# Kernel optimization log

Measured on AMD Instinct MI355X. Metric: run time of the kernel, lower is better.

Reference implementation:

```python
import jax, jax.numpy as jnp
import numpy as np

B, NP, K, E = 8, 4096, 1024, 262144   # graphs, nodes/graph, topk keep, edges
N = B * NP
EPS = 1e-5


def _glorot(k, fi, fo):
    lim = float(np.sqrt(6.0 / (fi + fo)))
    return jax.random.uniform(k, (fi, fo), jnp.float32, -lim, lim)


def setup_inputs() -> dict:
    key = jax.random.key(0)
    ks = jax.random.split(key, 16)
    pos = jax.random.normal(ks[0], (N, 3), jnp.float32)
    epg = E // B
    src = jax.random.randint(ks[1], (E,), 0, NP)
    dst = jax.random.randint(ks[2], (E,), 0, NP)
    off = jnp.repeat(jnp.arange(B) * NP, epg)   # edges stay within their graph
    edge_index = jnp.stack([src + off, dst + off]).astype(jnp.int32)
    batch = jnp.repeat(jnp.arange(B, dtype=jnp.int32), NP)
    inp = {"pos": pos, "edge_index": edge_index, "batch": batch,
           "p": jax.random.normal(ks[3], (3,), jnp.float32)}
    dims = [3, 64, 128, 128, 256, 512]
    for i in range(5):
        fi, fo = dims[i], dims[i + 1]
        inp[f"W{i+1}"] = _glorot(ks[4 + i], fi, fo)
        inp[f"b{i+1}"] = jnp.zeros((fo,), jnp.float32)
        inp[f"g{i+1}"] = jnp.ones((fo,), jnp.float32)
        inp[f"be{i+1}"] = jnp.zeros((fo,), jnp.float32)
    for i, (fi, fo) in enumerate([(512, 256), (256, 256), (256, 100)]):
        inp[f"fw{i+1}"] = _glorot(ks[9 + i], fi, fo)
        inp[f"fb{i+1}"] = jnp.zeros((fo,), jnp.float32)
    return inp


def _bn(x, g, b):
    # BatchNorm1d in training mode: batch stats over the node dim
    m = jnp.mean(x, 0)
    v = jnp.var(x, 0)
    return (x - m) * jax.lax.rsqrt(v + EPS) * g + b


def _gcn(x, src, dst, ew, W, bb, n):
    # GCNConv with add_self_loops=True, symmetric normalization.
    h = x @ W                                              # [n, out]
    deg = jax.ops.segment_sum(ew, dst, num_segments=n) + 1.0  # +1 self-loop
    dinv = jax.lax.rsqrt(deg)
    norm = dinv[src] * ew * dinv[dst]                      # masked edges -> 0
    agg = jax.ops.segment_sum(h[src] * norm[:, None], dst, num_segments=n)
    return agg + h * (dinv * dinv)[:, None] + bb           # self-loop term + bias


def _forward(pos, p, W1, b1, g1, be1, W2, b2, g2, be2, W3, b3, g3, be3,
             W4, b4, g4, be4, W5, b5, g5, be5, fw1, fb1, fw2, fb2, fw3, fb3,
             edge_index):
    # --- TopKPooling(ratio=1024): projection score, tanh, top-k per graph ---
    s = jnp.tanh(pos @ p / jnp.linalg.norm(p))             # [N]
    vals, idx = jax.lax.top_k(s.reshape(B, NP), K)         # [B,K]
    perm = (idx + (jnp.arange(B) * NP)[:, None]).reshape(-1)
    x = pos[perm] * vals.reshape(-1)[:, None]              # gate kept nodes
    Nn = B * K
    remap = jnp.full((N,), -1, jnp.int32).at[perm].set(jnp.arange(Nn, dtype=jnp.int32))
    src, dst = remap[edge_index[0]], remap[edge_index[1]]
    valid = (src >= 0) & (dst >= 0)
    ew = valid.astype(x.dtype)                             # 0-weight == removed edge
    src = jnp.where(valid, src, 0)
    dst = jnp.where(valid, dst, 0)
    for (W, bb, g, be) in ((W1, b1, g1, be1), (W2, b2, g2, be2),
                           (W3, b3, g3, be3), (W4, b4, g4, be4),
                           (W5, b5, g5, be5)):
        x = jax.nn.relu(_bn(_gcn(x, src, dst, ew, W, bb, Nn), g, be))
    # --- global sum pooling (torch_scatter default reduce='sum') ---
    batch_new = jnp.repeat(jnp.arange(B), K)
    x = jax.ops.segment_sum(x, batch_new, num_segments=B)  # [B,512]
    x = jax.nn.relu(x @ fw1 + fb1)
    x = jax.nn.relu(x @ fw2 + fb2)
    return jax.nn.log_softmax(x @ fw3 + fb3, axis=-1)      # [B,100]


def reference(pos, edge_index, batch, p, W1, b1, g1, be1, W2, b2, g2, be2,
              W3, b3, g3, be3, W4, b4, g4, be4, W5, b5, g5, be5,
              fw1, fb1, fw2, fb2, fw3, fb3):
    del batch  # graph ids are the fixed contiguous layout encoded in B, NP, K
    return _forward(pos, p, W1, b1, g1, be1, W2, b2, g2, be2, W3, b3, g3, be3,
                    W4, b4, g4, be4, W5, b5, g5, be5,
                    fw1, fb1, fw2, fb2, fw3, fb3, edge_index)
```

## Files before the change

### kernel.cpp

```cpp
#include <hip/hip_runtime.h>
#include <math.h>

#define NTOT 32768
#define NPG  4096
#define BGR  8
#define KK   1024
#define NN   8192
#define NE   262144

typedef __attribute__((ext_vector_type(8))) short bf16x8;
typedef __attribute__((ext_vector_type(4))) float f32x4;

static __device__ __forceinline__ unsigned short f2bf(float f) {
    unsigned u = __float_as_uint(f);
    return (unsigned short)((u + 0x7fffu + ((u >> 16) & 1u)) >> 16);
}
static __device__ __forceinline__ float bf2f(unsigned short b) {
    return __uint_as_float(((unsigned)b) << 16);
}

__global__ void k_init(int* remap, int* deg, int* cursor) {
    int i = blockIdx.x * blockDim.x + threadIdx.x;
    if (i < NTOT) remap[i] = -1;
    if (i < NN) { deg[i] = 0; cursor[i] = 0; }
}

__global__ __launch_bounds__(1024) void k_topk2(const float* __restrict__ pos,
                                                const float* __restrict__ p,
                                                int* __restrict__ remap,
                                                float* __restrict__ x0f,
                                                unsigned short* __restrict__ Ab0) {
    __shared__ unsigned skey[NPG];
    __shared__ float sval[NPG];
    __shared__ int hist[256];
    __shared__ int Sarr[256];
    __shared__ int wsum[16];
    __shared__ int s_bin, s_above;

    const int g = blockIdx.x, tid = threadIdx.x;
    const int lane = tid & 63, wid = tid >> 6;
    const float p0 = p[0], p1 = p[1], p2 = p[2];
    const float invn = 1.0f / sqrtf(p0 * p0 + p1 * p1 + p2 * p2);

    for (int i = tid; i < NPG; i += 1024) {
        const float* pp = pos + (size_t)(g * NPG + i) * 3;
        float s = tanhf((pp[0] * p0 + pp[1] * p1 + pp[2] * p2) * invn);
        sval[i] = s;
        unsigned b = __float_as_uint(s);
        skey[i] = (b & 0x80000000u) ? ~b : (b | 0x80000000u);
    }
    __syncthreads();

    unsigned prefix = 0;
    int needed = KK;
    for (int r = 0; r < 4; ++r) {
        const int sh = 24 - 8 * r;
        if (tid < 256) hist[tid] = 0;
        __syncthreads();
        for (int i = tid; i < NPG; i += 1024) {
            unsigned k = skey[i];
            bool act = (r == 0) || ((k >> (sh + 8)) == prefix);
            if (act) atomicAdd(&hist[(k >> sh) & 255u], 1);
        }
        __syncthreads();
        if (wid == 0) {
            int h0 = hist[4 * lane + 0], h1 = hist[4 * lane + 1];
            int h2 = hist[4 * lane + 2], h3 = hist[4 * lane + 3];
            int l3 = h3, l2 = h2 + l3, l1 = h1 + l2, l0 = h0 + l1;
            int t = l0;
            for (int off = 1; off < 64; off <<= 1) {
                int n = __shfl_down(t, off, 64);
                if (lane + off < 64) t += n;
            }
            int hi = t - l0;
            Sarr[4 * lane + 0] = l0 + hi;
            Sarr[4 * lane + 1] = l1 + hi;
            Sarr[4 * lane + 2] = l2 + hi;
            Sarr[4 * lane + 3] = l3 + hi;
        }
        __syncthreads();
        if (tid < 256) {
            int Sb = Sarr[tid];
            int Sb1 = (tid < 255) ? Sarr[tid + 1] : 0;
            if (Sb >= needed && Sb1 < needed) { s_bin = tid; s_above = Sb1; }
        }
        __syncthreads();
        needed -= s_above;
        prefix = (prefix << 8) | (unsigned)s_bin;
        __syncthreads();
    }
    const unsigned Tkey = prefix;
    const int needTies = needed;

    int tiebase = 0, keepbase = 0;
    for (int c = 0; c < 4; ++c) {
        const int i = c * 1024 + tid;
        const unsigned k = skey[i];
        const int tie = (k == Tkey) ? 1 : 0;
        int v = tie;
        for (int off = 1; off < 64; off <<= 1) {
            int n = __shfl_up(v, off, 64);
            if (lane >= off) v += n;
        }
        if (lane == 63) wsum[wid] = v;
        __syncthreads();
        if (wid == 0) {
            int w = (lane < 16) ? wsum[lane] : 0;
            for (int off = 1; off < 16; off <<= 1) {
                int n = __shfl_up(w, off, 64);
                if (lane >= off) w += n;
            }
            if (lane < 16) wsum[lane] = w;
        }
        __syncthreads();
        const int trank = tiebase + v + (wid > 0 ? wsum[wid - 1] : 0) - tie;
        const int ttot = wsum[15];
        const int keep = (k > Tkey) || (tie && trank < needTies);
        __syncthreads();
        int u = keep;
        for (int off = 1; off < 64; off <<= 1) {
            int n = __shfl_up(u, off, 64);
            if (lane >= off) u += n;
        }
        if (lane == 63) wsum[wid] = u;
        __syncthreads();
        if (wid == 0) {
            int w = (lane < 16) ? wsum[lane] : 0;
            for (int off = 1; off < 16; off <<= 1) {
                int n = __shfl_up(w, off, 64);
                if (lane >= off) w += n;
            }
            if (lane < 16) wsum[lane] = w;
        }
        __syncthreads();
        const int kincl = u + (wid > 0 ? wsum[wid - 1] : 0);
        const int ktot = wsum[15];
        if (keep) {
            int nn = g * KK + keepbase + kincl - 1;
            remap[g * NPG + i] = nn;
            float val = sval[i];
            const float* pp = pos + (size_t)(g * NPG + i) * 3;
            float v0 = pp[0] * val, v1 = pp[1] * val, v2 = pp[2] * val;
            x0f[(size_t)nn * 3 + 0] = v0;
            x0f[(size_t)nn * 3 + 1] = v1;
            x0f[(size_t)nn * 3 + 2] = v2;
            unsigned short* rw = Ab0 + (size_t)nn * 32;
            ushort4 a = make_ushort4(f2bf(v0), f2bf(v1), f2bf(v2), 0);
            ushort4 z = make_ushort4(0, 0, 0, 0);
            *(ushort4*)(rw) = a;
#pragma unroll
            for (int t = 1; t < 8; ++t) *(ushort4*)(rw + 4 * t) = z;
        }
        tiebase += ttot;
        keepbase += ktot;
        __syncthreads();
    }
}

__global__ void k_deg(const int* __restrict__ ei, const int* __restrict__ remap,
                      int* __restrict__ deg) {
    int e = blockIdx.x * blockDim.x + threadIdx.x;
    if (e >= NE) return;
    int s = remap[ei[e]];
    int d = remap[ei[NE + e]];
    if (s >= 0 && d >= 0) atomicAdd(&deg[d], 1);
}

__global__ __launch_bounds__(1024) void k_scan(const int* __restrict__ deg,
                                               int* __restrict__ rowptr) {
    __shared__ int part[1024];
    const int tid = threadIdx.x;
    const int base = tid * 8;
    int loc[8];
    int s = 0;
#pragma unroll
    for (int i = 0; i < 8; ++i) { loc[i] = s; s += deg[base + i]; }
    part[tid] = s;
    __syncthreads();
    for (int off = 1; off < 1024; off <<= 1) {
        int v = (tid >= off) ? part[tid - off] : 0;
        __syncthreads();
        part[tid] += v;
        __syncthreads();
    }
    int pre = (tid > 0) ? part[tid - 1] : 0;
#pragma unroll
    for (int i = 0; i < 8; ++i) rowptr[base + i] = pre + loc[i];
    if (tid == 1023) rowptr[NN] = pre + s;
}

__global__ void k_place2(const int* __restrict__ ei, const int* __restrict__ remap,
                         const int* __restrict__ deg, const int* __restrict__ rowptr,
                         int* __restrict__ cursor, int* __restrict__ col,
                         float* __restrict__ ew) {
    int e = blockIdx.x * blockDim.x + threadIdx.x;
    if (e >= NE) return;
    int s = remap[ei[e]];
    int d = remap[ei[NE + e]];
    if (s >= 0 && d >= 0) {
        int pos = rowptr[d] + atomicAdd(&cursor[d], 1);
        col[pos] = s;
        ew[pos] = rsqrtf((float)(deg[s] + 1)) * rsqrtf((float)(deg[d] + 1));
    }
}

__global__ void k_wt_all(const float* __restrict__ w0, const float* __restrict__ w1,
                         const float* __restrict__ w2, const float* __restrict__ w3,
                         const float* __restrict__ w4,
                         unsigned short* __restrict__ t0, unsigned short* __restrict__ t1,
                         unsigned short* __restrict__ t2, unsigned short* __restrict__ t3,
                         unsigned short* __restrict__ t4) {
    int i = blockIdx.x * blockDim.x + threadIdx.x;
    const float* W; unsigned short* T; int Kd, Nc, Kpad, base;
    if (i < 2048)        { W = w0; T = t0; Kd = 3;   Nc = 64;  Kpad = 32;  base = 0; }
    else if (i < 10240)  { W = w1; T = t1; Kd = 64;  Nc = 128; Kpad = 64;  base = 2048; }
    else if (i < 26624)  { W = w2; T = t2; Kd = 128; Nc = 128; Kpad = 128; base = 10240; }
    else if (i < 59392)  { W = w3; T = t3; Kd = 128; Nc = 256; Kpad = 128; base = 26624; }
    else if (i < 190464) { W = w4; T = t4; Kd = 256; Nc = 512; Kpad = 256; base = 59392; }
    else return;
    int j = i - base;
    int n = j / Kpad, k = j - n * Kpad;
    float v = (k < Kd) ? W[(size_t)k * Nc + n] : 0.0f;
    T[j] = f2bf(v);
}

__global__ __launch_bounds__(256) void k_mm2(const unsigned short* __restrict__ Ab,
                                             const float* __restrict__ Yin,
                                             const float* __restrict__ scale,
                                             const float* __restrict__ shift,
                                             const unsigned short* __restrict__ WT,
                                             unsigned short* __restrict__ Hb,
                                             int Kd, int Nc) {
    const int lane = threadIdx.x & 63, wid = threadIdx.x >> 6;
    const int bm = blockIdx.x * 64 + (wid >> 1) * 32;
    const int bn = blockIdx.y * 64 + (wid & 1) * 32;
    const int fr = lane & 15;
    const int ko = (lane >> 4) << 3;
    const int row0 = bm + fr;
    const unsigned short* B0 = WT + (size_t)(bn + fr) * Kd + ko;
    const size_t strA = (size_t)16 * Kd;
    f32x4 acc00 = {0,0,0,0}, acc01 = {0,0,0,0}, acc10 = {0,0,0,0}, acc11 = {0,0,0,0};
    for (int k0 = 0; k0 < Kd; k0 += 32) {
        bf16x8 a0, a1;
        if (Yin) {
            const int cc = ko + k0;
            const float4 sc0 = *(const float4*)&scale[cc];
            const float4 sc1 = *(const float4*)&scale[cc + 4];
            const float4 sh0 = *(const float4*)&shift[cc];
            const float4 sh1 = *(const float4*)&shift[cc + 4];
            const float* y0 = Yin + (size_t)row0 * Kd + cc;
            const float* y1 = y0 + strA;
#pragma unroll
            for (int h = 0; h < 2; ++h) {
                const float* yy = h ? y1 : y0;
                float4 u = *(const float4*)yy;
                float4 v = *(const float4*)(yy + 4);
                float r0 = fmaxf(u.x * sc0.x + sh0.x, 0.0f);
                float r1 = fmaxf(u.y * sc0.y + sh0.y, 0.0f);
                float r2 = fmaxf(u.z * sc0.z + sh0.z, 0.0f);
                float r3 = fmaxf(u.w * sc0.w + sh0.w, 0.0f);
                float r4 = fmaxf(v.x * sc1.x + sh1.x, 0.0f);
                float r5 = fmaxf(v.y * sc1.y + sh1.y, 0.0f);
                float r6 = fmaxf(v.z * sc1.z + sh1.z, 0.0f);
                float r7 = fmaxf(v.w * sc1.w + sh1.w, 0.0f);
                bf16x8 a;
                a[0] = (short)f2bf(r0); a[1] = (short)f2bf(r1);
                a[2] = (short)f2bf(r2); a[3] = (short)f2bf(r3);
                a[4] = (short)f2bf(r4); a[5] = (short)f2bf(r5);
                a[6] = (short)f2bf(r6); a[7] = (short)f2bf(r7);
                if (h) a1 = a; else a0 = a;
            }
        } else {
            const unsigned short* A0 = Ab + (size_t)row0 * Kd + ko + k0;
            a0 = *(const bf16x8*)A0;
            a1 = *(const bf16x8*)(A0 + strA);
        }
        bf16x8 b0 = *(const bf16x8*)(B0 + k0);
        bf16x8 b1 = *(const bf16x8*)(B0 + strA + k0);
        acc00 = __builtin_amdgcn_mfma_f32_16x16x32_bf16(b0, a0, acc00, 0, 0, 0);
        acc01 = __builtin_amdgcn_mfma_f32_16x16x32_bf16(b1, a0, acc01, 0, 0, 0);
        acc10 = __builtin_amdgcn_mfma_f32_16x16x32_bf16(b0, a1, acc10, 0, 0, 0);
        acc11 = __builtin_amdgcn_mfma_f32_16x16x32_bf16(b1, a1, acc11, 0, 0, 0);
    }
    const int r = lane & 15;
    const int c4 = (lane >> 4) << 2;
#pragma unroll
    for (int tm = 0; tm < 2; ++tm) {
        const int row = bm + tm * 16 + r;
        const size_t basep = (size_t)row * Nc;
        const f32x4 aL = tm ? acc10 : acc00;
        const f32x4 aR = tm ? acc11 : acc01;
#pragma unroll
        for (int tn = 0; tn < 2; ++tn) {
            const f32x4 a = tn ? aR : aL;
            const int c = bn + tn * 16 + c4;
            *(ushort4*)&Hb[basep + c] = make_ushort4(f2bf(a[0]), f2bf(a[1]),
                                                     f2bf(a[2]), f2bf(a[3]));
        }
    }
}

#define BM 64
#define BNT 64
#define BKT 16
__global__ __launch_bounds__(256) void k_mm(const float* __restrict__ A,
                                            const float* __restrict__ W,
                                            float* __restrict__ H, int Kd, int Nc) {
    __shared__ float As[BM][BKT + 1];
    __shared__ float Bs[BKT][BNT + 1];
    const int bm = blockIdx.x * BM;
    const int bn = blockIdx.y * BNT;
    const int tid = threadIdx.x;
    const int tx = tid & 15, ty = tid >> 4;
    float acc[4][4] = {};
    for (int k0 = 0; k0 < Kd; k0 += BKT) {
        for (int t = 0; t < 4; ++t) {
            int i = tid + t * 256;
            int m = i >> 4, k = i & 15;
            As[m][k] = (k0 + k < Kd) ? A[(size_t)(bm + m) * Kd + k0 + k] : 0.0f;
        }
        for (int t = 0; t < 4; ++t) {
            int i = tid + t * 256;
            int k = i >> 6, n = i & 63;
            Bs[k][n] = (k0 + k < Kd) ? W[(size_t)(k0 + k) * Nc + bn + n] : 0.0f;
        }
        __syncthreads();
        for (int k = 0; k < BKT; ++k) {
            float a[4], b[4];
#pragma unroll
            for (int i = 0; i < 4; ++i) a[i] = As[ty * 4 + i][k];
#pragma unroll
            for (int j = 0; j < 4; ++j) b[j] = Bs[k][tx * 4 + j];
#pragma unroll
            for (int i = 0; i < 4; ++i)
#pragma unroll
                for (int j = 0; j < 4; ++j) acc[i][j] += a[i] * b[j];
        }
        __syncthreads();
    }
#pragma unroll
    for (int i = 0; i < 4; ++i)
        *(float4*)&H[(size_t)(bm + ty * 4 + i) * Nc + bn + tx * 4] =
            make_float4(acc[i][0], acc[i][1], acc[i][2], acc[i][3]);
}

#define BN1_ROWS 16
#define BN1_CHUNKS (NN / BN1_ROWS)
__global__ __launch_bounds__(256) void k_gfuse(const unsigned short* __restrict__ Hb,
                                               const float* __restrict__ Hf,
                                               const int* __restrict__ rowptr,
                                               const int* __restrict__ col,
                                               const float* __restrict__ ew,
                                               const int* __restrict__ deg,
                                               const float* __restrict__ bias,
                                               float* __restrict__ Y,
                                               float* __restrict__ psum,
                                               float* __restrict__ psq, int Nc) {
    __shared__ float4 ls[256], lq[256];
    const int CHB = (Nc < 128) ? Nc : 128;
    const int CB = Nc / CHB;
    const int chunk = blockIdx.x / CB;
    const int cb = blockIdx.x - chunk * CB;
    const int QPB = CHB >> 2;
    const int tid = threadIdx.x;
    const int q = tid & (QPB - 1);
    const int rg = tid / QPB;
    const int NRG = 256 / QPB;
    const int RPT = BN1_ROWS / NRG;
    const int c = cb * CHB + (q << 2);
    const float4 b4 = *(const float4*)&bias[c];
    float4 s4 = make_float4(0, 0, 0, 0), q4 = make_float4(0, 0, 0, 0);
    for (int rr = 0; rr < RPT; ++rr) {
        const int n = chunk * BN1_ROWS + rg * RPT + rr;
        const int j0 = rowptr[n], j1 = rowptr[n + 1];
        const float inv = 1.0f / (float)(deg[n] + 1);
        float4 acc;
        if (Hb) {
            ushort4 hv = *(const ushort4*)&Hb[(size_t)n * Nc + c];
            acc = make_float4(bf2f(hv.x), bf2f(hv.y), bf2f(hv.z), bf2f(hv.w));
        } else {
            acc = *(const float4*)&Hf[(size_t)n * Nc + c];
        }
        acc.x = acc.x * inv + b4.x;
        acc.y = acc.y * inv + b4.y;
        acc.z = acc.z * inv + b4.z;
        acc.w = acc.w * inv + b4.w;
        if (Hb) {
            for (int j = j0; j < j1; ++j) {
                const float w = ew[j];
                ushort4 hv = *(const ushort4*)&Hb[(size_t)col[j] * Nc + c];
                acc.x += bf2f(hv.x) * w; acc.y += bf2f(hv.y) * w;
                acc.z += bf2f(hv.z) * w; acc.w += bf2f(hv.w) * w;
            }
        } else {
            for (int j = j0; j < j1; ++j) {
                const float w = ew[j];
                const float4 hv = *(const float4*)&Hf[(size_t)col[j] * Nc + c];
                acc.x += hv.x * w; acc.y += hv.y * w; acc.z += hv.z * w; acc.w += hv.w * w;
            }
        }
        *(float4*)&Y[(size_t)n * Nc + c] = acc;
        s4.x += acc.x; s4.y += acc.y; s4.z += acc.z; s4.w += acc.w;
        q4.x += acc.x * acc.x; q4.y += acc.y * acc.y;
        q4.z += acc.z * acc.z; q4.w += acc.w * acc.w;
    }
    ls[tid] = s4; lq[tid] = q4;
    __syncthreads();
    for (int st = 128; st >= QPB; st >>= 1) {
        if (tid < st) {
            float4 a = ls[tid], b = ls[tid + st];
            ls[tid] = make_float4(a.x + b.x, a.y + b.y, a.z + b.z, a.w + b.w);
            float4 e = lq[tid], f = lq[tid + st];
            lq[tid] = make_float4(e.x + f.x, e.y + f.y, e.z + f.z, e.w + f.w);
        }
        __syncthreads();
    }
    if (tid < QPB) {
        *(float4*)&psum[(size_t)chunk * Nc + c] = ls[tid];
        *(float4*)&psq[(size_t)chunk * Nc + c] = lq[tid];
    }
}

__global__ __launch_bounds__(256) void k_bn2p(const float* __restrict__ psum,
                                              const float* __restrict__ psq,
                                              const float* __restrict__ g,
                                              const float* __restrict__ be,
                                              float* __restrict__ scale,
                                              float* __restrict__ shift, int Nc) {
    __shared__ float ss[256], sq[256];
    const int c = blockIdx.x;
    const int t = threadIdx.x;
    float s = 0.0f, q = 0.0f;
    for (int b = t; b < BN1_CHUNKS; b += 256) {
        s += psum[(size_t)b * Nc + c];
        q += psq[(size_t)b * Nc + c];
    }
    ss[t] = s; sq[t] = q;
    __syncthreads();
    for (int st = 128; st > 0; st >>= 1) {
        if (t < st) { ss[t] += ss[t + st]; sq[t] += sq[t + st]; }
        __syncthreads();
    }
    if (t == 0) {
        double mean = (double)ss[0] / 8192.0;
        double var = (double)sq[0] / 8192.0 - mean * mean;
        float sc = (float)((double)g[c] / sqrt(var + 1e-5));
        scale[c] = sc;
        shift[c] = be[c] - (float)mean * sc;
    }
}

__global__ void k_bnapply(float* x, const float* __restrict__ scale,
                          const float* __restrict__ shift, int Nc) {
    int i = blockIdx.x * blockDim.x + threadIdx.x;
    int c4 = i & ((Nc >> 2) - 1);
    float4 v = ((const float4*)x)[i];
    float4 sc = ((const float4*)scale)[c4];
    float4 sh = ((const float4*)shift)[c4];
    v.x = fmaxf(v.x * sc.x + sh.x, 0.0f);
    v.y = fmaxf(v.y * sc.y + sh.y, 0.0f);
    v.z = fmaxf(v.z * sc.z + sh.z, 0.0f);
    v.w = fmaxf(v.w * sc.w + sh.w, 0.0f);
    ((float4*)x)[i] = v;
}

#define PR 32
__global__ __launch_bounds__(256) void k_pool_af(const float* __restrict__ Y,
                                                 const float* __restrict__ scale,
                                                 const float* __restrict__ shift,
                                                 float* __restrict__ part) {
    __shared__ float4 red[128];
    const int g = blockIdx.x >> 5;
    const int rs = blockIdx.x & 31;
    const int half = threadIdx.x >> 7;
    const int q = threadIdx.x & 127;
    const float4 sc = *(const float4*)&scale[4 * q];
    const float4 sh = *(const float4*)&shift[4 * q];
    const float* xp = Y + (size_t)(g * KK + rs * PR + half * 16) * 512 + 4 * q;
    float4 s = make_float4(0, 0, 0, 0);
#pragma unroll
    for (int rr = 0; rr < 16; ++rr) {
        float4 v = *(const float4*)(xp + (size_t)rr * 512);
        s.x += fmaxf(v.x * sc.x + sh.x, 0.0f);
        s.y += fmaxf(v.y * sc.y + sh.y, 0.0f);
        s.z += fmaxf(v.z * sc.z + sh.z, 0.0f);
        s.w += fmaxf(v.w * sc.w + sh.w, 0.0f);
    }
    if (half == 1) red[q] = s;
    __syncthreads();
    if (half == 0) {
        float4 t = red[q];
        s.x += t.x; s.y += t.y; s.z += t.z; s.w += t.w;
        *(float4*)&part[(size_t)blockIdx.x * 512 + 4 * q] = s;
    }
}

__global__ __launch_bounds__(256) void k_pool(const float* __restrict__ x, float* pooled) {
    __shared__ float red[4][64];
    int g = blockIdx.x >> 3;
    int c0 = (blockIdx.x & 7) * 64;
    int c = threadIdx.x & 63;
    int rp = threadIdx.x >> 6;
    float s = 0;
    for (int r = rp; r < KK; r += 4)
        s += x[(size_t)(g * KK + r) * 512 + c0 + c];
    red[rp][c] = s;
    __syncthreads();
    if (rp == 0)
        pooled[g * 512 + c0 + c] = red[0][c] + red[1][c] + red[2][c] + red[3][c];
}

__global__ __launch_bounds__(256) void k_fc1(const float* __restrict__ part,
                                             const float* __restrict__ fw1,
                                             const float* __restrict__ fb1,
                                             float* __restrict__ t1, int nparts) {
    __shared__ float pooled[512];
    const int g = blockIdx.x, tid = threadIdx.x;
    for (int c = tid; c < 512; c += 256) {
        float s = 0;
        for (int i = 0; i < nparts; ++i) s += part[(size_t)(g * nparts + i) * 512 + c];
        pooled[c] = s;
    }
    __syncthreads();
    float acc = fb1[tid];
    for (int k = 0; k < 512; ++k) acc += pooled[k] * fw1[k * 256 + tid];
    t1[g * 256 + tid] = acc > 0.0f ? acc : 0.0f;
}

__global__ void k_fc(const float* __restrict__ in, const float* __restrict__ W,
                     const float* __restrict__ bias, float* out, int fi, int fo) {
    __shared__ float row[512];
    int g = blockIdx.x, tid = threadIdx.x;
    for (int k = tid; k < fi; k += blockDim.x) row[k] = in[g * fi + k];
    __syncthreads();
    if (tid < fo) {
        float acc = bias[tid];
        for (int k = 0; k < fi; ++k) acc += row[k] * W[k * fo + tid];
        out[g * fo + tid] = acc > 0.0f ? acc : 0.0f;
    }
}

__global__ __launch_bounds__(256) void k_fc23(const float* __restrict__ t1,
                                              const float* __restrict__ fw2,
                                              const float* __restrict__ fb2,
                                              const float* __restrict__ fw3,
                                              const float* __restrict__ fb3,
                                              float* __restrict__ out) {
    __shared__ float row[256];
    __shared__ float t2s[256];
    __shared__ float red[256];
    __shared__ float logits[100];
    const int g = blockIdx.x, tid = threadIdx.x;
    row[tid] = t1[g * 256 + tid];
    __syncthreads();
    float acc = fb2[tid];
    for (int k = 0; k < 256; ++k) acc += row[k] * fw2[k * 256 + tid];
    t2s[tid] = acc > 0.0f ? acc : 0.0f;
    __syncthreads();
    float v = -INFINITY;
    if (tid < 100) {
        float a3 = fb3[tid];
        for (int k = 0; k < 256; ++k) a3 += t2s[k] * fw3[k * 100 + tid];
        logits[tid] = a3;
        v = a3;
    }
    red[tid] = v;
    __syncthreads();
    for (int s = 128; s > 0; s >>= 1) {
        if (tid < s) red[tid] = fmaxf(red[tid], red[tid + s]);
        __syncthreads();
    }
    float mx = red[0];
    __syncthreads();
    red[tid] = (tid < 100) ? expf(logits[tid] - mx) : 0.0f;
    __syncthreads();
    for (int s = 128; s > 0; s >>= 1) {
        if (tid < s) red[tid] += red[tid + s];
        __syncthreads();
    }
    float lse = logf(red[0]);
    if (tid < 100) out[g * 100 + tid] = logits[tid] - mx - lse;
}

extern "C" void kernel_launch(void* const* d_in, const int* in_sizes, int n_in,
                              void* d_out, int out_size, void* d_ws, size_t ws_size,
                              hipStream_t stream) {
    const float* pos = (const float*)d_in[0];
    const int* ei = (const int*)d_in[1];
    const float* p = (const float*)d_in[3];
    const float *W[5], *bb[5], *gg[5], *be[5];
    for (int i = 0; i < 5; ++i) {
        W[i]  = (const float*)d_in[4 + 4 * i];
        bb[i] = (const float*)d_in[5 + 4 * i];
        gg[i] = (const float*)d_in[6 + 4 * i];
        be[i] = (const float*)d_in[7 + 4 * i];
    }
    const float* fw1 = (const float*)d_in[24]; const float* fb1 = (const float*)d_in[25];
    const float* fw2 = (const float*)d_in[26]; const float* fb2 = (const float*)d_in[27];
    const float* fw3 = (const float*)d_in[28]; const float* fb3 = (const float*)d_in[29];
    float* out = (float*)d_out;

    const int fins[5]  = {3, 64, 128, 128, 256};
    const int kpads[5] = {32, 64, 128, 128, 256};
    const int fouts[5] = {64, 128, 128, 256, 512};

    size_t off = 0;
    char* base = (char*)d_ws;
    auto alloc = [&](size_t bytes) { char* q = base + off; off += (bytes + 255) & ~(size_t)255; return q; };

    float* Y      = (float*)alloc((size_t)NN * 512 * 4);
    float* Hf     = (float*)alloc((size_t)NN * 512 * 4);
    int*   remap  = (int*)alloc((size_t)NTOT * 4);
    int*   deg    = (int*)alloc(NN * 4);
    int*   cursor = (int*)alloc(NN * 4);
    int*   rowptr = (int*)alloc((NN + 1) * 4);
    int*   ecol   = (int*)alloc((size_t)NE * 4);
    float* ew     = (float*)alloc((size_t)NE * 4);
    float* psum   = (float*)alloc((size_t)BN1_CHUNKS * 512 * 4);
    float* psq    = (float*)alloc((size_t)BN1_CHUNKS * 512 * 4);
    float* scale  = (float*)alloc(512 * 4);
    float* shift  = (float*)alloc(512 * 4);
    float* pooled = (float*)alloc(8 * 512 * 4);
    float* t1     = (float*)alloc(8 * 256 * 4);
    unsigned short* Ab0 = (unsigned short*)alloc((size_t)NN * 32 * 2);
    float* part   = (float*)alloc((size_t)256 * 512 * 4);
    unsigned short* WT[5];
    for (int l = 0; l < 5; ++l) WT[l] = (unsigned short*)alloc((size_t)fouts[l] * kpads[l] * 2);
    unsigned short* Hb = (unsigned short*)Hf;
    const bool mfma = (ws_size >= off);

    k_init<<<NTOT / 256, 256, 0, stream>>>(remap, deg, cursor);
    k_topk2<<<BGR, 1024, 0, stream>>>(pos, p, remap, Y, Ab0);
    k_deg<<<NE / 256, 256, 0, stream>>>(ei, remap, deg);
    k_scan<<<1, 1024, 0, stream>>>(deg, rowptr);
    k_place2<<<NE / 256, 256, 0, stream>>>(ei, remap, deg, rowptr, cursor, ecol, ew);

    if (mfma) {
        k_wt_all<<<(190464 + 255) / 256, 256, 0, stream>>>(W[0], W[1], W[2], W[3], W[4],
                                                           WT[0], WT[1], WT[2], WT[3], WT[4]);
        for (int l = 0; l < 5; ++l) {
            int fo = fouts[l];
            dim3 mg(NN / 64, fo / 64);
            if (l == 0)
                k_mm2<<<mg, 256, 0, stream>>>(Ab0, nullptr, nullptr, nullptr,
                                              WT[l], Hb, kpads[l], fo);
            else
                k_mm2<<<mg, 256, 0, stream>>>(nullptr, Y, scale, shift,
                                              WT[l], Hb, kpads[l], fo);
            int cbs = (fo < 128) ? 1 : fo / 128;
            k_gfuse<<<BN1_CHUNKS * cbs, 256, 0, stream>>>(Hb, nullptr, rowptr, ecol, ew,
                                                          deg, bb[l], Y, psum, psq, fo);
            k_bn2p<<<fo, 256, 0, stream>>>(psum, psq, gg[l], be[l], scale, shift, fo);
        }
        k_pool_af<<<256, 256, 0, stream>>>(Y, scale, shift, part);
        k_fc1<<<8, 256, 0, stream>>>(part, fw1, fb1, t1, 32);
        k_fc23<<<8, 256, 0, stream>>>(t1, fw2, fb2, fw3, fb3, out);
    } else {
        for (int l = 0; l < 5; ++l) {
            int fi = fins[l], fo = fouts[l];
            dim3 mg(NN / BM, fo / BNT);
            k_mm<<<mg, 256, 0, stream>>>(Y, W[l], Hf, fi, fo);
            int cbs = (fo < 128) ? 1 : fo / 128;
            k_gfuse<<<BN1_CHUNKS * cbs, 256, 0, stream>>>(nullptr, Hf, rowptr, ecol, ew,
                                                          deg, bb[l], Y, psum, psq, fo);
            k_bn2p<<<fo, 256, 0, stream>>>(psum, psq, gg[l], be[l], scale, shift, fo);
            k_bnapply<<<(NN * fo) / 1024, 256, 0, stream>>>(Y, scale, shift, fo);
        }
        k_pool<<<64, 256, 0, stream>>>(Y, pooled);
        k_fc<<<8, 256, 0, stream>>>(pooled, fw1, fb1, t1, 512, 256);
        k_fc23<<<8, 256, 0, stream>>>(t1, fw2, fb2, fw3, fb3, out);
    }
}
```

Before: 218.2 us.

## Fuse BN stats via atomics, merge init/FC kernels, stage A tile in LDS

Removes k_init by folding the deg/cursor/remap initialisation into k_topk2 and the gstat zeroing into k_deg. Replaces the per-chunk psum/psq partials plus the k_bn2p reduction kernel with float atomics into a per-layer gstat buffer. Each consumer kernel (k_mm2, k_pool_af, k_bnapply) now recomputes the BN scale and shift itself. k_mm2 stages the normalised A tile once in shared memory and loops over all output column tiles, and k_fc1/k_fc23 are merged into one kernel. Together these cut the launch count per layer and avoid re-normalising A for each column block, at the cost of atomic contention, a less deterministic summation order and fewer blocks in the GEMM grid.

Result: slower. 317.3 us (+45.4%).

```diff
diff --git a/kernel.cpp b/kernel.cpp
--- a/kernel.cpp
+++ b/kernel.cpp
@@ -19,17 +19,13 @@
     return __uint_as_float(((unsigned)b) << 16);
 }
 
-__global__ void k_init(int* remap, int* deg, int* cursor) {
-    int i = blockIdx.x * blockDim.x + threadIdx.x;
-    if (i < NTOT) remap[i] = -1;
-    if (i < NN) { deg[i] = 0; cursor[i] = 0; }
-}
-
 __global__ __launch_bounds__(1024) void k_topk2(const float* __restrict__ pos,
                                                 const float* __restrict__ p,
                                                 int* __restrict__ remap,
                                                 float* __restrict__ x0f,
-                                                unsigned short* __restrict__ Ab0) {
+                                                unsigned short* __restrict__ Ab0,
+                                                int* __restrict__ deg,
+                                                int* __restrict__ cursor) {
     __shared__ unsigned skey[NPG];
     __shared__ float sval[NPG];
     __shared__ int hist[256];
@@ -39,6 +35,8 @@
 
     const int g = blockIdx.x, tid = threadIdx.x;
     const int lane = tid & 63, wid = tid >> 6;
+    deg[g * KK + tid] = 0;
+    cursor[g * KK + tid] = 0;
     const float p0 = p[0], p1 = p[1], p2 = p[2];
     const float invn = 1.0f / sqrtf(p0 * p0 + p1 * p1 + p2 * p2);
 
@@ -150,6 +148,8 @@
             *(ushort4*)(rw) = a;
 #pragma unroll
             for (int t = 1; t < 8; ++t) *(ushort4*)(rw + 4 * t) = z;
+        } else {
+            remap[g * NPG + i] = -1;
         }
         tiebase += ttot;
         keepbase += ktot;
@@ -158,8 +158,9 @@
 }
 
 __global__ void k_deg(const int* __restrict__ ei, const int* __restrict__ remap,
-                      int* __restrict__ deg) {
+                      int* __restrict__ deg, float* __restrict__ gstatAll) {
     int e = blockIdx.x * blockDim.x + threadIdx.x;
+    if (e < 5 * 1024) gstatAll[e] = 0.0f;
     if (e >= NE) return;
     int s = remap[ei[e]];
     int d = remap[ei[NE + e]];
@@ -224,78 +225,88 @@
     T[j] = f2bf(v);
 }
 
-__global__ __launch_bounds__(256) void k_mm2(const unsigned short* __restrict__ Ab,
+#define KPAD_MAX 264
+__global__ __launch_bounds__(256) void k_mm2(const unsigned short* __restrict__ Ab0,
                                              const float* __restrict__ Yin,
-                                             const float* __restrict__ scale,
-                                             const float* __restrict__ shift,
+                                             const float* __restrict__ gstat,
+                                             const float* __restrict__ gamma,
+                                             const float* __restrict__ beta,
                                              const unsigned short* __restrict__ WT,
                                              unsigned short* __restrict__ Hb,
                                              int Kd, int Nc) {
-    const int lane = threadIdx.x & 63, wid = threadIdx.x >> 6;
-    const int bm = blockIdx.x * 64 + (wid >> 1) * 32;
-    const int bn = blockIdx.y * 64 + (wid & 1) * 32;
+    __shared__ unsigned short As[64 * KPAD_MAX];
+    __shared__ float sc_s[256], sh_s[256];
+    const int tid = threadIdx.x;
+    const int bm = blockIdx.x * 64;
+    const int KP = Kd + 8;
+    const int QK = Kd >> 2;
+    if (Yin) {
+        for (int c = tid; c < Kd; c += 256) {
+            double mean = (double)gstat[c] / 8192.0;
+            double var = (double)gstat[512 + c] / 8192.0 - mean * mean;
+            float sc = (float)((double)gamma[c] / sqrt(var + 1e-5));
+            sc_s[c] = sc;
+            sh_s[c] = beta[c] - (float)mean * sc;
+        }
+        __syncthreads();
+        for (int idx = tid; idx < 64 * QK; idx += 256) {
+            int row = idx / QK, q = idx - row * QK;
+            float4 v = *(const float4*)&Yin[(size_t)(bm + row) * Kd + 4 * q];
+            float4 sc = *(const float4*)&sc_s[4 * q];
+            float4 sh = *(const float4*)&sh_s[4 * q];
+            ushort4 o;
+            o.x = f2bf(fmaxf(v.x * sc.x + sh.x, 0.0f));
+            o.y = f2bf(fmaxf(v.y * sc.y + sh.y, 0.0f));
+            o.z = f2bf(fmaxf(v.z * sc.z + sh.z, 0.0f));
+            o.w = f2bf(fmaxf(v.w * sc.w + sh.w, 0.0f));
+            *(ushort4*)&As[row * KP + 4 * q] = o;
+        }
+    } else {
+        for (int idx = tid; idx < 64 * QK; idx += 256) {
+            int row = idx / QK, q = idx - row * QK;
+            *(ushort4*)&As[row * KP + 4 * q] =
+                *(const ushort4*)&Ab0[(size_t)(bm + row) * Kd + 4 * q];
+        }
+    }
+    __syncthreads();
+
+    const int lane = tid & 63, wid = tid >> 6;
+    const int rloc = (wid >> 1) * 32;
+    const int cloc = (wid & 1) * 32;
     const int fr = lane & 15;
     const int ko = (lane >> 4) << 3;
-    const int row0 = bm + fr;
-    const unsigned short* B0 = WT + (size_t)(bn + fr) * Kd + ko;
-    const size_t strA = (size_t)16 * Kd;
-    f32x4 acc00 = {0,0,0,0}, acc01 = {0,0,0,0}, acc10 = {0,0,0,0}, acc11 = {0,0,0,0};
-    for (int k0 = 0; k0 < Kd; k0 += 32) {
-        bf16x8 a0, a1;
-        if (Yin) {
-            const int cc = ko + k0;
-            const float4 sc0 = *(const float4*)&scale[cc];
-            const float4 sc1 = *(const float4*)&scale[cc + 4];
-            const float4 sh0 = *(const float4*)&shift[cc];
-            const float4 sh1 = *(const float4*)&shift[cc + 4];
-            const float* y0 = Yin + (size_t)row0 * Kd + cc;
-            const float* y1 = y0 + strA;
-#pragma unroll
-            for (int h = 0; h < 2; ++h) {
-                const float* yy = h ? y1 : y0;
-                float4 u = *(const float4*)yy;
-                float4 v = *(const float4*)(yy + 4);
-                float r0 = fmaxf(u.x * sc0.x + sh0.x, 0.0f);
-                float r1 = fmaxf(u.y * sc0.y + sh0.y, 0.0f);
-                float r2 = fmaxf(u.z * sc0.z + sh0.z, 0.0f);
-                float r3 = fmaxf(u.w * sc0.w + sh0.w, 0.0f);
-                float r4 = fmaxf(v.x * sc1.x + sh1.x, 0.0f);
-                float r5 = fmaxf(v.y * sc1.y + sh1.y, 0.0f);
-                float r6 = fmaxf(v.z * sc1.z + sh1.z, 0.0f);
-                float r7 = fmaxf(v.w * sc1.w + sh1.w, 0.0f);
-                bf16x8 a;
-                a[0] = (short)f2bf(r0); a[1] = (short)f2bf(r1);
-                a[2] = (short)f2bf(r2); a[3] = (short)f2bf(r3);
-                a[4] = (short)f2bf(r4); a[5] = (short)f2bf(r5);
-                a[6] = (short)f2bf(r6); a[7] = (short)f2bf(r7);
-                if (h) a1 = a; else a0 = a;
-            }
-        } else {
-            const unsigned short* A0 = Ab + (size_t)row0 * Kd + ko + k0;
-            a0 = *(const bf16x8*)A0;
-            a1 = *(const bf16x8*)(A0 + strA);
-        }
-        bf16x8 b0 = *(const bf16x8*)(B0 + k0);
-        bf16x8 b1 = *(const bf16x8*)(B0 + strA + k0);
-        acc00 = __builtin_amdgcn_mfma_f32_16x16x32_bf16(b0, a0, acc00, 0, 0, 0);
-        acc01 = __builtin_amdgcn_mfma_f32_16x16x32_bf16(b1, a0, acc01, 0, 0, 0);
-        acc10 = __builtin_amdgcn_mfma_f32_16x16x32_bf16(b0, a1, acc10, 0, 0, 0);
-        acc11 = __builtin_amdgcn_mfma_f32_16x16x32_bf16(b1, a1, acc11, 0, 0, 0);
-    }
+    const unsigned short* A0 = &As[(rloc + fr) * KP + ko];
+    const int strA = 16 * KP;
+    const size_t strB = (size_t)16 * Kd;
     const int r = lane & 15;
     const int c4 = (lane >> 4) << 2;
-#pragma unroll
-    for (int tm = 0; tm < 2; ++tm) {
-        const int row = bm + tm * 16 + r;
-        const size_t basep = (size_t)row * Nc;
-        const f32x4 aL = tm ? acc10 : acc00;
-        const f32x4 aR = tm ? acc11 : acc01;
-#pragma unroll
-        for (int tn = 0; tn < 2; ++tn) {
-            const f32x4 a = tn ? aR : aL;
-            const int c = bn + tn * 16 + c4;
-            *(ushort4*)&Hb[basep + c] = make_ushort4(f2bf(a[0]), f2bf(a[1]),
-                                                     f2bf(a[2]), f2bf(a[3]));
+
+    for (int ct = 0; ct < Nc; ct += 64) {
+        const unsigned short* B0 = WT + (size_t)(ct + cloc + fr) * Kd + ko;
+        f32x4 acc00 = {0,0,0,0}, acc01 = {0,0,0,0}, acc10 = {0,0,0,0}, acc11 = {0,0,0,0};
+        for (int k0 = 0; k0 < Kd; k0 += 32) {
+            bf16x8 a0 = *(const bf16x8*)(A0 + k0);
+            bf16x8 a1 = *(const bf16x8*)(A0 + strA + k0);
+            bf16x8 b0 = *(const bf16x8*)(B0 + k0);
+            bf16x8 b1 = *(const bf16x8*)(B0 + strB + k0);
+            acc00 = __builtin_amdgcn_mfma_f32_16x16x32_bf16(b0, a0, acc00, 0, 0, 0);
+            acc01 = __builtin_amdgcn_mfma_f32_16x16x32_bf16(b1, a0, acc01, 0, 0, 0);
+            acc10 = __builtin_amdgcn_mfma_f32_16x16x32_bf16(b0, a1, acc10, 0, 0, 0);
+            acc11 = __builtin_amdgcn_mfma_f32_16x16x32_bf16(b1, a1, acc11, 0, 0, 0);
+        }
+#pragma unroll
+        for (int tm = 0; tm < 2; ++tm) {
+            const int row = bm + rloc + tm * 16 + r;
+            const size_t basep = (size_t)row * Nc;
+            const f32x4 aL = tm ? acc10 : acc00;
+            const f32x4 aR = tm ? acc11 : acc01;
+#pragma unroll
+            for (int tn = 0; tn < 2; ++tn) {
+                const f32x4 a = tn ? aR : aL;
+                const int c = ct + cloc + tn * 16 + c4;
+                *(ushort4*)&Hb[basep + c] = make_ushort4(f2bf(a[0]), f2bf(a[1]),
+                                                         f2bf(a[2]), f2bf(a[3]));
+            }
         }
     }
 }
@@ -344,7 +355,7 @@
             make_float4(acc[i][0], acc[i][1], acc[i][2], acc[i][3]);
 }
 
-#define BN1_ROWS 16
+#define BN1_ROWS 32
 #define BN1_CHUNKS (NN / BN1_ROWS)
 __global__ __launch_bounds__(256) void k_gfuse(const unsigned short* __restrict__ Hb,
                                                const float* __restrict__ Hf,
@@ -354,24 +365,20 @@
                                                const int* __restrict__ deg,
                                                const float* __restrict__ bias,
                                                float* __restrict__ Y,
-                                               float* __restrict__ psum,
-                                               float* __restrict__ psq, int Nc) {
+                                               float* __restrict__ gstat, int Nc) {
     __shared__ float4 ls[256], lq[256];
-    const int CHB = (Nc < 128) ? Nc : 128;
-    const int CB = Nc / CHB;
+    const int CB = Nc >> 6;
     const int chunk = blockIdx.x / CB;
     const int cb = blockIdx.x - chunk * CB;
-    const int QPB = CHB >> 2;
     const int tid = threadIdx.x;
-    const int q = tid & (QPB - 1);
-    const int rg = tid / QPB;
-    const int NRG = 256 / QPB;
-    const int RPT = BN1_ROWS / NRG;
-    const int c = cb * CHB + (q << 2);
+    const int q = tid & 15;
+    const int rg = tid >> 4;
+    const int c = cb * 64 + (q << 2);
     const float4 b4 = *(const float4*)&bias[c];
     float4 s4 = make_float4(0, 0, 0, 0), q4 = make_float4(0, 0, 0, 0);
-    for (int rr = 0; rr < RPT; ++rr) {
-        const int n = chunk * BN1_ROWS + rg * RPT + rr;
+#pragma unroll
+    for (int rr = 0; rr < 2; ++rr) {
+        const int n = chunk * BN1_ROWS + rg * 2 + rr;
         const int j0 = rowptr[n], j1 = rowptr[n + 1];
         const float inv = 1.0f / (float)(deg[n] + 1);
         float4 acc;
@@ -406,7 +413,7 @@
     }
     ls[tid] = s4; lq[tid] = q4;
     __syncthreads();
-    for (int st = 128; st >= QPB; st >>= 1) {
+    for (int st = 128; st >= 16; st >>= 1) {
         if (tid < st) {
             float4 a = ls[tid], b = ls[tid + st];
             ls[tid] = make_float4(a.x + b.x, a.y + b.y, a.z + b.z, a.w + b.w);
@@ -415,68 +422,66 @@
         }
         __syncthreads();
     }
-    if (tid < QPB) {
-        *(float4*)&psum[(size_t)chunk * Nc + c] = ls[tid];
-        *(float4*)&psq[(size_t)chunk * Nc + c] = lq[tid];
-    }
-}
-
-__global__ __launch_bounds__(256) void k_bn2p(const float* __restrict__ psum,
-                                              const float* __restrict__ psq,
-                                              const float* __restrict__ g,
-                                              const float* __restrict__ be,
-                                              float* __restrict__ scale,
-                                              float* __restrict__ shift, int Nc) {
-    __shared__ float ss[256], sq[256];
-    const int c = blockIdx.x;
-    const int t = threadIdx.x;
-    float s = 0.0f, q = 0.0f;
-    for (int b = t; b < BN1_CHUNKS; b += 256) {
-        s += psum[(size_t)b * Nc + c];
-        q += psq[(size_t)b * Nc + c];
-    }
-    ss[t] = s; sq[t] = q;
-    __syncthreads();
-    for (int st = 128; st > 0; st >>= 1) {
-        if (t < st) { ss[t] += ss[t + st]; sq[t] += sq[t + st]; }
-        __syncthreads();
-    }
-    if (t == 0) {
-        double mean = (double)ss[0] / 8192.0;
-        double var = (double)sq[0] / 8192.0 - mean * mean;
-        float sc = (float)((double)g[c] / sqrt(var + 1e-5));
-        scale[c] = sc;
-        shift[c] = be[c] - (float)mean * sc;
-    }
-}
-
-__global__ void k_bnapply(float* x, const float* __restrict__ scale,
-                          const float* __restrict__ shift, int Nc) {
+    if (tid < 16) {
+        float4 a = ls[tid], b = lq[tid];
+        atomicAdd(&gstat[c + 0], a.x); atomicAdd(&gstat[c + 1], a.y);
+        atomicAdd(&gstat[c + 2], a.z); atomicAdd(&gstat[c + 3], a.w);
+        atomicAdd(&gstat[512 + c + 0], b.x); atomicAdd(&gstat[512 + c + 1], b.y);
+        atomicAdd(&gstat[512 + c + 2], b.z); atomicAdd(&gstat[512 + c + 3], b.w);
+    }
+}
+
+__global__ void k_bnapply(float* x, const float* __restrict__ gstat,
+                          const float* __restrict__ gamma, const float* __restrict__ beta,
+                          int Nc) {
     int i = blockIdx.x * blockDim.x + threadIdx.x;
-    int c4 = i & ((Nc >> 2) - 1);
+    int c0 = (i & ((Nc >> 2) - 1)) << 2;
     float4 v = ((const float4*)x)[i];
-    float4 sc = ((const float4*)scale)[c4];
-    float4 sh = ((const float4*)shift)[c4];
-    v.x = fmaxf(v.x * sc.x + sh.x, 0.0f);
-    v.y = fmaxf(v.y * sc.y + sh.y, 0.0f);
-    v.z = fmaxf(v.z * sc.z + sh.z, 0.0f);
-    v.w = fmaxf(v.w * sc.w + sh.w, 0.0f);
-    ((float4*)x)[i] = v;
+    float r[4] = {v.x, v.y, v.z, v.w};
+#pragma unroll
+    for (int k = 0; k < 4; ++k) {
+        int c = c0 + k;
+        double mean = (double)gstat[c] / 8192.0;
+        double var = (double)gstat[512 + c] / 8192.0 - mean * mean;
+        float sc = (float)((double)gamma[c] / sqrt(var + 1e-5));
+        float sh = beta[c] - (float)mean * sc;
+        r[k] = fmaxf(r[k] * sc + sh, 0.0f);
+    }
+    ((float4*)x)[i] = make_float4(r[0], r[1], r[2], r[3]);
 }
 
 #define PR 32
 __global__ __launch_bounds__(256) void k_pool_af(const float* __restrict__ Y,
-                                                 const float* __restrict__ scale,
-                                                 const float* __restrict__ shift,
+                                                 const float* __restrict__ gstat,
+                                                 const float* __restrict__ gamma,
+                                                 const float* __restrict__ beta,
                                                  float* __restrict__ part) {
     __shared__ float4 red[128];
     const int g = blockIdx.x >> 5;
     const int rs = blockIdx.x & 31;
     const int half = threadIdx.x >> 7;
     const int q = threadIdx.x & 127;
-    const float4 sc = *(const float4*)&scale[4 * q];
-    const float4 sh = *(const float4*)&shift[4 * q];
-    const float* xp = Y + (size_t)(g * KK + rs * PR + half * 16) * 512 + 4 * q;
+    const int c = 4 * q;
+    float4 sc, sh;
+    {
+        double m0 = (double)gstat[c + 0] / 8192.0;
+        double v0 = (double)gstat[512 + c + 0] / 8192.0 - m0 * m0;
+        sc.x = (float)((double)gamma[c + 0] / sqrt(v0 + 1e-5));
+        sh.x = beta[c + 0] - (float)m0 * sc.x;
+        double m1 = (double)gstat[c + 1] / 8192.0;
+        double v1 = (double)gstat[512 + c + 1] / 8192.0 - m1 * m1;
+        sc.y = (float)((double)gamma[c + 1] / sqrt(v1 + 1e-5));
+        sh.y = beta[c + 1] - (float)m1 * sc.y;
+        double m2 = (double)gstat[c + 2] / 8192.0;
+        double v2 = (double)gstat[512 + c + 2] / 8192.0 - m2 * m2;
+        sc.z = (float)((double)gamma[c + 2] / sqrt(v2 + 1e-5));
+        sh.z = beta[c + 2] - (float)m2 * sc.z;
+        double m3 = (double)gstat[c + 3] / 8192.0;
+        double v3 = (double)gstat[512 + c + 3] / 8192.0 - m3 * m3;
+        sc.w = (float)((double)gamma[c + 3] / sqrt(v3 + 1e-5));
+        sh.w = beta[c + 3] - (float)m3 * sc.w;
+    }
+    const float* xp = Y + (size_t)(g * KK + rs * PR + half * 16) * 512 + c;
     float4 s = make_float4(0, 0, 0, 0);
 #pragma unroll
     for (int rr = 0; rr < 16; ++rr) {
@@ -491,7 +496,7 @@
     if (half == 0) {
         float4 t = red[q];
         s.x += t.x; s.y += t.y; s.z += t.z; s.w += t.w;
-        *(float4*)&part[(size_t)blockIdx.x * 512 + 4 * q] = s;
+        *(float4*)&part[(size_t)blockIdx.x * 512 + c] = s;
     }
 }
 
@@ -510,11 +515,19 @@
         pooled[g * 512 + c0 + c] = red[0][c] + red[1][c] + red[2][c] + red[3][c];
 }
 
-__global__ __launch_bounds__(256) void k_fc1(const float* __restrict__ part,
-                                             const float* __restrict__ fw1,
-                                             const float* __restrict__ fb1,
-                                             float* __restrict__ t1, int nparts) {
+__global__ __launch_bounds__(256) void k_fc123(const float* __restrict__ part,
+                                               const float* __restrict__ fw1,
+                                               const float* __restrict__ fb1,
+                                               const float* __restrict__ fw2,
+                                               const float* __restrict__ fb2,
+                                               const float* __restrict__ fw3,
+                                               const float* __restrict__ fb3,
+                                               float* __restrict__ out, int nparts) {
     __shared__ float pooled[512];
+    __shared__ float t1s[256];
+    __shared__ float t2s[256];
+    __shared__ float red[256];
+    __shared__ float logits[100];
     const int g = blockIdx.x, tid = threadIdx.x;
     for (int c = tid; c < 512; c += 256) {
         float s = 0;
@@ -522,9 +535,37 @@
         pooled[c] = s;
     }
     __syncthreads();
-    float acc = fb1[tid];
-    for (int k = 0; k < 512; ++k) acc += pooled[k] * fw1[k * 256 + tid];
-    t1[g * 256 + tid] = acc > 0.0f ? acc : 0.0f;
+    float a1 = fb1[tid];
+    for (int k = 0; k < 512; ++k) a1 += pooled[k] * fw1[k * 256 + tid];
+    t1s[tid] = fmaxf(a1, 0.0f);
+    __syncthreads();
+    float a2 = fb2[tid];
+    for (int k = 0; k < 256; ++k) a2 += t1s[k] * fw2[k * 256 + tid];
+    t2s[tid] = fmaxf(a2, 0.0f);
+    __syncthreads();
+    float v = -INFINITY;
+    if (tid < 100) {
+        float a3 = fb3[tid];
+        for (int k = 0; k < 256; ++k) a3 += t2s[k] * fw3[k * 100 + tid];
+        logits[tid] = a3;
+        v = a3;
+    }
+    red[tid] = v;
+    __syncthreads();
+    for (int s = 128; s > 0; s >>= 1) {
+        if (tid < s) red[tid] = fmaxf(red[tid], red[tid + s]);
+        __syncthreads();
+    }
+    float mx = red[0];
+    __syncthreads();
+    red[tid] = (tid < 100) ? expf(logits[tid] - mx) : 0.0f;
+    __syncthreads();
+    for (int s = 128; s > 0; s >>= 1) {
+        if (tid < s) red[tid] += red[tid + s];
+        __syncthreads();
+    }
+    float lse = logf(red[0]);
+    if (tid < 100) out[g * 100 + tid] = logits[tid] - mx - lse;
 }
 
 __global__ void k_fc(const float* __restrict__ in, const float* __restrict__ W,
@@ -616,10 +657,7 @@
     int*   rowptr = (int*)alloc((NN + 1) * 4);
     int*   ecol   = (int*)alloc((size_t)NE * 4);
     float* ew     = (float*)alloc((size_t)NE * 4);
-    float* psum   = (float*)alloc((size_t)BN1_CHUNKS * 512 * 4);
-    float* psq    = (float*)alloc((size_t)BN1_CHUNKS * 512 * 4);
-    float* scale  = (float*)alloc(512 * 4);
-    float* shift  = (float*)alloc(512 * 4);
+    float* gstat  = (float*)alloc(5 * 1024 * 4);
     float* pooled = (float*)alloc(8 * 512 * 4);
     float* t1     = (float*)alloc(8 * 256 * 4);
     unsigned short* Ab0 = (unsigned short*)alloc((size_t)NN * 32 * 2);
@@ -629,9 +667,8 @@
     unsigned short* Hb = (unsigned short*)Hf;
     const bool mfma = (ws_size >= off);
 
-    k_init<<<NTOT / 256, 256, 0, stream>>>(remap, deg, cursor);
-    k_topk2<<<BGR, 1024, 0, stream>>>(pos, p, remap, Y, Ab0);
-    k_deg<<<NE / 256, 256, 0, stream>>>(ei, remap, deg);
+    k_topk2<<<BGR, 1024, 0, stream>>>(pos, p, remap, Y, Ab0, deg, cursor);
+    k_deg<<<NE / 256, 256, 0, stream>>>(ei, remap, deg, gstat);
     k_scan<<<1, 1024, 0, stream>>>(deg, rowptr);
     k_place2<<<NE / 256, 256, 0, stream>>>(ei, remap, deg, rowptr, cursor, ecol, ew);
 
@@ -640,31 +677,29 @@
                                                            WT[0], WT[1], WT[2], WT[3], WT[4]);
         for (int l = 0; l < 5; ++l) {
             int fo = fouts[l];
-            dim3 mg(NN / 64, fo / 64);
             if (l == 0)
-                k_mm2<<<mg, 256, 0, stream>>>(Ab0, nullptr, nullptr, nullptr,
-                                              WT[l], Hb, kpads[l], fo);
+                k_mm2<<<NN / 64, 256, 0, stream>>>(Ab0, nullptr, nullptr, nullptr, nullptr,
+                                                   WT[l], Hb, kpads[l], fo);
             else
-                k_mm2<<<mg, 256, 0, stream>>>(nullptr, Y, scale, shift,
-                                              WT[l], Hb, kpads[l], fo);
-            int cbs = (fo < 128) ? 1 : fo / 128;
-            k_gfuse<<<BN1_CHUNKS * cbs, 256, 0, stream>>>(Hb, nullptr, rowptr, ecol, ew,
-                                                          deg, bb[l], Y, psum, psq, fo);
-            k_bn2p<<<fo, 256, 0, stream>>>(psum, psq, gg[l], be[l], scale, shift, fo);
-        }
-        k_pool_af<<<256, 256, 0, stream>>>(Y, scale, shift, part);
-        k_fc1<<<8, 256, 0, stream>>>(part, fw1, fb1, t1, 32);
-        k_fc23<<<8, 256, 0, stream>>>(t1, fw2, fb2, fw3, fb3, out);
+                k_mm2<<<NN / 64, 256, 0, stream>>>(nullptr, Y, gstat + (l - 1) * 1024,
+                                                   gg[l - 1], be[l - 1],
+                                                   WT[l], Hb, kpads[l], fo);
+            k_gfuse<<<BN1_CHUNKS * (fo >> 6), 256, 0, stream>>>(Hb, nullptr, rowptr, ecol, ew,
+                                                                deg, bb[l], Y,
+                                                                gstat + l * 1024, fo);
+        }
+        k_pool_af<<<256, 256, 0, stream>>>(Y, gstat + 4 * 1024, gg[4], be[4], part);
+        k_fc123<<<8, 256, 0, stream>>>(part, fw1, fb1, fw2, fb2, fw3, fb3, out, 32);
     } else {
         for (int l = 0; l < 5; ++l) {
             int fi = fins[l], fo = fouts[l];
             dim3 mg(NN / BM, fo / BNT);
             k_mm<<<mg, 256, 0, stream>>>(Y, W[l], Hf, fi, fo);
-            int cbs = (fo < 128) ? 1 : fo / 128;
-            k_gfuse<<<BN1_CHUNKS * cbs, 256, 0, stream>>>(nullptr, Hf, rowptr, ecol, ew,
-                                                          deg, bb[l], Y, psum, psq, fo);
-            k_bn2p<<<fo, 256, 0, stream>>>(psum, psq, gg[l], be[l], scale, shift, fo);
-            k_bnapply<<<(NN * fo) / 1024, 256, 0, stream>>>(Y, scale, shift, fo);
+            k_gfuse<<<BN1_CHUNKS * (fo >> 6), 256, 0, stream>>>(nullptr, Hf, rowptr, ecol, ew,
+                                                                deg, bb[l], Y,
+                                                                gstat + l * 1024, fo);
+            k_bnapply<<<(NN * fo) / 1024, 256, 0, stream>>>(Y, gstat + l * 1024,
+                                                            gg[l], be[l], fo);
         }
         k_pool<<<64, 256, 0, stream>>>(Y, pooled);
         k_fc<<<8, 256, 0, stream>>>(pooled, fw1, fb1, t1, 512, 256);
```
